# Kernel optimization log

Measured on AMD Instinct MI355X. Metric: run time of the kernel, lower is better.

The kernel has to match this reference:

```python
import jax, jax.numpy as jnp
import numpy as np

H = 128            # hardcoded image side in the torch module
TOL = 1e-3         # forward() default tol
MAX_DEPTH = 8      # init kwarg (reduced from 200 for bounded runtime)
LRELU = 0.1        # LeakyReLU negative slope


def _conv(x, w, b, pad):
    # x: [B,Cin,H,H], w: [Cout,Cin,kh,kw]
    y = jax.lax.conv_general_dilated(
        x, w, (1, 1), [(pad, pad), (pad, pad)],
        dimension_numbers=('NCHW', 'OIHW', 'NCHW'))
    if b is not None:
        y = y + b[None, :, None, None]
    return y


def _leaky(x):
    return jnp.where(x >= 0, x, LRELU * x)


def _build_apply_T(d, A, w1, b1, w2, b2, w3, b3, wK, delta, alpha, lambd, beta):
    B = d.shape[0]
    Kc = wK.shape[0]
    dcol = d.reshape(B, -1).T                      # [m, B]
    # ConvTranspose2d(K->1, k=3, pad=1) with weight := convK.weight is the
    # adjoint of convK: regular conv with spatially flipped, channel-swapped kernel.
    wKt = jnp.transpose(jnp.flip(wK, (2, 3)), (1, 0, 2, 3))  # [1,K,3,3]

    def K_op(xk):                                  # [N,B] -> [K*N,B]
        x4 = xk.T.reshape(B, 1, H, H)
        return _conv(x4, wK, None, 1).reshape(B, -1).T

    def Kt_op(pk):                                 # [K*N,B] -> [N,B]
        p4 = pk.T.reshape(B, Kc, H, H)
        return _conv(p4, wKt, None, 1).reshape(B, -1).T

    def R_op(pk):                                  # learned residual denoiser
        p = pk.T.reshape(B, Kc, H, H)
        p = p + _leaky(_conv(p, w1, b1, 2))
        p = p + _leaky(_conv(p, w2, b2, 2))
        p = p + _leaky(_conv(p, w3, b3, 2))
        return p.reshape(B, -1).T

    def ball_proj(w):                              # eval-mode projection
        de = jnp.exp(delta)                        # (1,) -> broadcasts over batch
        dist = jnp.maximum(jnp.linalg.norm(w - dcol, axis=0), 1e-10)
        dn = jnp.linalg.norm(dcol, axis=0)
        scale = jnp.minimum(jnp.ones_like(dist), de * dn / dist)
        return dcol + scale * (w - dcol)

    a = jnp.clip(alpha, 0.0, 2.0)
    bta = jnp.clip(beta, 0.0, 2.0)
    lam = jnp.clip(lambd, 0.0, 2.0)

    def apply_T(x):                                # x: [B,1,H,H]
        xk = x.reshape(B, -1).T                    # [N,B]
        Kxk = K_op(xk)
        # torch: pk = K(xk); pk += lambd*(nuk1 + alpha*(K(xk)-pk)) with nuk1=0
        # and pk==K(xk), so the update is identity -> pk = Kxk.
        pk = R_op(Kxk)
        Axk = A @ xk                               # [m,B]
        # torch: wk = A@xk; temp = wk + lambd*(nuk2 + alpha*(Axk-wk)) = Axk.
        wk = ball_proj(Axk)
        nuk1p = a * (Kxk - pk)
        nuk2p = a * (Axk - wk)
        # nuk1 = nuk2 = 0, so 2*nuk_plus - nuk = 2*nuk_plus
        rk = Kt_op(2.0 * nuk1p) + A.T @ (2.0 * nuk2p)
        xk_new = jnp.clip(xk - bta * rk, 0.0, 1.0)
        return xk_new.T.reshape(B, 1, H, H)

    return apply_T


def setup_inputs() -> dict:
    key = jax.random.key(0)
    ks = jax.random.split(key, 10)
    B, M, N_side, Kc = 8, 4096, 128, 2
    d = jax.random.normal(ks[0], (B, M), jnp.float32)
    A = jax.random.normal(ks[1], (M, N_side * N_side), jnp.float32) / 128.0
    w1 = jax.random.normal(ks[2], (Kc, Kc, 5, 5), jnp.float32) * 0.05
    w2 = jax.random.normal(ks[3], (Kc, Kc, 5, 5), jnp.float32) * 0.05
    w3 = jax.random.normal(ks[4], (Kc, Kc, 5, 5), jnp.float32) * 0.05
    b1 = jnp.zeros((Kc,), jnp.float32)
    b2 = jnp.zeros((Kc,), jnp.float32)
    b3 = jnp.zeros((Kc,), jnp.float32)
    wK = jax.random.normal(ks[5], (Kc, 1, 3, 3), jnp.float32) * 0.1
    return {
        'd': d, 'A': A,
        'w1': w1, 'b1': b1, 'w2': w2, 'b2': b2, 'w3': w3, 'b3': b3,
        'wK': wK,
        'delta': jnp.full((1,), -5.0, jnp.float32),
        'alpha': jnp.full((1,), 0.1, jnp.float32),
        'lambd': jnp.full((1,), 0.1, jnp.float32),
        'beta': jnp.full((1,), 0.1, jnp.float32),
    }


def reference(d, A, w1, b1, w2, b2, w3, b3, wK, delta, alpha, lambd, beta):
    B = d.shape[0]
    apply_T = _build_apply_T(d, A, w1, b1, w2, b2, w3, b3, wK,
                             delta, alpha, lambd, beta)
    x0 = jnp.zeros((B, 1, H, H), d.dtype)
    xp0 = jnp.full((B, 1, H, H), jnp.inf, d.dtype)

    def cond(state):
        x, xp, k = state
        res = jnp.max(jnp.linalg.norm((x - xp).reshape(B, -1), axis=1))
        return (res > TOL) & (k < MAX_DEPTH)

    def body(state):
        x, xp, k = state
        return (apply_T(x), x, k + 1)

    x_star, _, _ = jax.lax.while_loop(cond, body, (x0, xp0, jnp.int32(0)))
    # final differentiable application T(x*)
    return apply_T(x_star)
```

## Files before the change

### kernel.cpp

```cpp
#include <hip/hip_runtime.h>
#include <math.h>

#define HH 128
#define NPIX 16384
#define BB 8
#define MM 4096
#define NN 16384
#define LRELU_S 0.1f

typedef __attribute__((ext_vector_type(8))) short bf16x8;
typedef __attribute__((ext_vector_type(4))) float f32x4;

__device__ __forceinline__ float leaky_(float v){ return v >= 0.f ? v : LRELU_S*v; }
__device__ __forceinline__ float clamp01(float v){ return fminf(fmaxf(v, 0.f), 1.f); }
__device__ __forceinline__ float clamp02(float v){ return fminf(fmaxf(v, 0.f), 2.f); }
__device__ __forceinline__ unsigned short f2bf(float f){
  unsigned u = __float_as_uint(f);
  u = (u + 0x7FFFu + ((u >> 16) & 1u)) >> 16;
  return (unsigned short)u;
}
__device__ __forceinline__ float bf2f(unsigned short s){
  return __uint_as_float(((unsigned)s) << 16);
}

__global__ __launch_bounds__(256) void k_prep_both(const float* __restrict__ A_,
                                                   unsigned short* __restrict__ Abf,
                                                   unsigned short* __restrict__ Apk){
  __shared__ unsigned short lb[16][1032];
  int blk = blockIdx.x;
  int mt = blk >> 4, ch = blk & 15;
  int t = threadIdx.x;
  #pragma unroll
  for (int i=0;i<16;++i){
    float4 v = *(const float4*)&A_[(size_t)(mt*16+i)*NN + ch*1024 + t*4];
    unsigned short o[4] = {f2bf(v.x),f2bf(v.y),f2bf(v.z),f2bf(v.w)};
    *(uint2*)&lb[i][t*4] = *(uint2*)o;
    *(uint2*)&Abf[(size_t)(mt*16+i)*NN + ch*1024 + t*4] = *(uint2*)o;
  }
  __syncthreads();
  size_t base = ((size_t)mt*2048 + ch*128)*128;
  #pragma unroll
  for (int j=0;j<8;++j){
    int o = j*256 + t;
    int k8l = o >> 4, col = o & 15;
    uint4 v = *(const uint4*)&lb[col][k8l*8];
    *(uint4*)&Apk[base + (size_t)o*8] = v;
  }
}

__global__ __launch_bounds__(256) void k_dn(const float* __restrict__ d, float* __restrict__ dn){
  int b = blockIdx.x, t = threadIdx.x;
  float ss = 0.f;
  for (int m=t; m<MM; m+=256){ float v = d[b*MM + m]; ss += v*v; }
  #pragma unroll
  for (int off=32; off; off>>=1) ss += __shfl_down(ss, off);
  __shared__ float red[4];
  if ((t & 63) == 0) red[t>>6] = ss;
  __syncthreads();
  if (t == 0) dn[b] = sqrtf(red[0]+red[1]+red[2]+red[3]);
}

__global__ __launch_bounds__(256) void k_gemm1p(const unsigned short* __restrict__ Apk,
    const unsigned short* __restrict__ xtt, float* __restrict__ e_part){
  __shared__ float part[4][16][16];
  int blk = blockIdx.x;
  int mt = blk >> 2, ng = blk & 3;
  int t = threadIdx.x, w = t >> 6, lane = t & 63;
  int kg = lane >> 4, col = lane & 15;
  const unsigned short* Ap = Apk + (((size_t)mt*2048 + ng*512 + w*128 + kg)*16 + col)*8;
  const unsigned short* Bp = xtt + ((size_t)(ng*512 + w*128 + kg)*16 + col)*8;
  f32x4 acc = {0.f,0.f,0.f,0.f};
  #pragma unroll 8
  for (int s=0; s<32; ++s){
    bf16x8 a = *(const bf16x8*)(Ap + s*512);
    bf16x8 b = *(const bf16x8*)(Bp + s*512);
    acc = __builtin_amdgcn_mfma_f32_16x16x32_bf16(a, b, acc, 0, 0, 0);
  }
  #pragma unroll
  for (int j=0;j<4;++j) part[w][kg*4+j][col] = acc[j];
  __syncthreads();
  int r = t >> 4, b = t & 15;
  float s = part[0][r][b] + part[1][r][b] + part[2][r][b] + part[3][r][b];
  e_part[((size_t)ng*MM + mt*16 + r)*16 + b] = s;
}

__global__ __launch_bounds__(256) void k_conv_chain(const float* __restrict__ x,
    const float* __restrict__ wK, const float* __restrict__ w1, const float* __restrict__ b1,
    const float* __restrict__ w2, const float* __restrict__ b2,
    const float* __restrict__ w3, const float* __restrict__ b3,
    const float* __restrict__ alpha, float* __restrict__ rk){
  __shared__ float xs[24][128];
  __shared__ float bufA[2][22][128];
  __shared__ float bufB[2][18][128];
  __shared__ float wKs[18], w1s[100], w2s[100], w3s[100], bs[3][2];
  __shared__ float twoa;
  int blk = blockIdx.x;
  int b = blk >> 4, slab = blk & 15, r0 = slab*8;
  int t = threadIdx.x;
  for (int i=t;i<18;i+=256) wKs[i]=wK[i];
  for (int i=t;i<100;i+=256){ w1s[i]=w1[i]; w2s[i]=w2[i]; w3s[i]=w3[i]; }
  if (t<2){ bs[0][t]=b1[t]; bs[1][t]=b2[t]; bs[2][t]=b3[t]; }
  if (t==0) twoa = 2.f*clamp02(alpha[0]);
  for (int idx=t; idx<24*128; idx+=256){
    int i = idx>>7, j = idx&127, ir = r0-8+i;
    xs[i][j] = ((unsigned)ir < 128u) ? x[b*NPIX + ir*HH + j] : 0.f;
  }
  __syncthreads();
  for (int c=0;c<2;++c)
    for (int idx=t; idx<22*128; idx+=256){
      int i = idx>>7, j = idx&127, ir = r0-7+i;
      float s = 0.f;
      if ((unsigned)ir < 128u){
        #pragma unroll
        for (int di=0;di<3;++di)
          #pragma unroll
          for (int dj=0;dj<3;++dj){
            int jj = j+dj-1;
            if ((unsigned)jj < 128u) s += xs[i+di][jj]*wKs[(c*3+di)*3+dj];
          }
      }
      bufA[c][i][j] = s;
    }
  __syncthreads();
  for (int o=0;o<2;++o)
    for (int idx=t; idx<18*128; idx+=256){
      int i = idx>>7, j = idx&127, ir = r0-5+i;
      float v = 0.f;
      if ((unsigned)ir < 128u){
        float s = bs[0][o];
        #pragma unroll
        for (int c=0;c<2;++c)
          #pragma unroll
          for (int di=0;di<5;++di)
            #pragma unroll
            for (int dj=0;dj<5;++dj){
              int jj = j+dj-2;
              if ((unsigned)jj < 128u) s += bufA[c][i+di][jj]*w1s[(o*2+c)*25+di*5+dj];
            }
        v = bufA[o][i+2][j] + leaky_(s);
      }
      bufB[o][i][j] = v;
    }
  __syncthreads();
  for (int o=0;o<2;++o)
    for (int idx=t; idx<14*128; idx+=256){
      int i = idx>>7, j = idx&127, ir = r0-3+i;
      float v = 0.f;
      if ((unsigned)ir < 128u){
        float s = bs[1][o];
        #pragma unroll
        for (int c=0;c<2;++c)
          #pragma unroll
          for (int di=0;di<5;++di)
            #pragma unroll
            for (int dj=0;dj<5;++dj){
              int jj = j+dj-2;
              if ((unsigned)jj < 128u) s += bufB[c][i+di][jj]*w2s[(o*2+c)*25+di*5+dj];
            }
        v = bufB[o][i+2][j] + leaky_(s);
      }
      bufA[o][i][j] = v;
    }
  __syncthreads();
  for (int o=0;o<2;++o)
    for (int idx=t; idx<10*128; idx+=256){
      int i = idx>>7, j = idx&127, ir = r0-1+i;
      float v = 0.f;
      if ((unsigned)ir < 128u){
        float s = bs[2][o];
        #pragma unroll
        for (int c=0;c<2;++c)
          #pragma unroll
          for (int di=0;di<5;++di)
            #pragma unroll
            for (int dj=0;dj<5;++dj){
              int jj = j+dj-2;
              if ((unsigned)jj < 128u) s += bufA[c][i+di][jj]*w3s[(o*2+c)*25+di*5+dj];
            }
        v = bufA[o][i+2][j] + leaky_(s);
      }
      bufB[o][i][j] = v;
    }
  __syncthreads();
  for (int c=0;c<2;++c)
    for (int idx=t; idx<10*128; idx+=256){
      int i = idx>>7, j = idx&127, ir = r0-1+i;
      float v = 0.f;
      if ((unsigned)ir < 128u){
        float kx = 0.f;
        #pragma unroll
        for (int di=0;di<3;++di)
          #pragma unroll
          for (int dj=0;dj<3;++dj){
            int jj = j+dj-1;
            if ((unsigned)jj < 128u) kx += xs[i+6+di][jj]*wKs[(c*3+di)*3+dj];
          }
        v = twoa*(kx - bufB[c][i][j]);
      }
      bufA[c][i][j] = v;
    }
  __syncthreads();
  for (int idx=t; idx<8*128; idx+=256){
    int i = idx>>7, j = idx&127, ir = r0+i;
    float s = 0.f;
    #pragma unroll
    for (int c=0;c<2;++c)
      #pragma unroll
      for (int di=0;di<3;++di)
        #pragma unroll
        for (int dj=0;dj<3;++dj){
          int jj = j+dj-1;
          if ((unsigned)jj < 128u) s += bufA[c][i+di][jj]*wKs[(c*3+(2-di))*3+(2-dj)];
        }
    rk[b*NPIX + ir*HH + j] = s;
  }
}

__global__ __launch_bounds__(256) void k_gemm2n(const unsigned short* __restrict__ Abf,
    const float* __restrict__ e_part, const float* __restrict__ d_,
    float* __restrict__ up, float* __restrict__ d2p){
  __shared__ float zs[8][128];
  __shared__ float red8s[64];
  int blk = blockIdx.x;
  int ms = blk >> 5, nb = blk & 31;
  int m0 = ms*128, n0 = nb*512;
  int t = threadIdx.x;
  for (int i=t; i<1024; i+=256){
    int ml = i >> 3, b = i & 7;
    int m = m0 + ml;
    float s = e_part[(size_t)(0*MM + m)*16 + b]
            + e_part[(size_t)(1*MM + m)*16 + b]
            + e_part[(size_t)(2*MM + m)*16 + b]
            + e_part[(size_t)(3*MM + m)*16 + b];
    zs[b][ml] = s - d_[b*MM + m];
  }
  __syncthreads();
  if (nb == 0){
    if (t < 64){
      int b = t & 7, g = t >> 3;
      float s = 0.f;
      #pragma unroll
      for (int i=0;i<16;++i){ float v = zs[b][g*16+i]; s += v*v; }
      red8s[g*8 + b] = s;
    }
    __syncthreads();
    if (t < 8){
      float s2 = 0.f;
      #pragma unroll
      for (int g=0;g<8;++g) s2 += red8s[g*8 + t];
      d2p[ms*8 + t] = s2;
    }
  }
  int c = t & 127, h = t >> 7;
  const unsigned short* Ap = Abf + (size_t)(m0 + h*64)*NN + n0 + c*4;
  float acc[4][8];
  #pragma unroll
  for (int e=0;e<4;++e)
    #pragma unroll
    for (int b=0;b<8;++b) acc[e][b] = 0.f;
  for (int mo=0; mo<64; mo+=8){
    uint2 a8[8];
    #pragma unroll
    for (int u=0;u<8;++u) a8[u] = *(const uint2*)(Ap + (size_t)(mo+u)*NN);
    #pragma unroll
    for (int u=0;u<8;++u){
      float av0 = bf2f((unsigned short)(a8[u].x & 0xffff));
      float av1 = bf2f((unsigned short)(a8[u].x >> 16));
      float av2 = bf2f((unsigned short)(a8[u].y & 0xffff));
      float av3 = bf2f((unsigned short)(a8[u].y >> 16));
      int ml = h*64 + mo + u;
      #pragma unroll
      for (int b=0;b<8;++b){
        float z = zs[b][ml];
        acc[0][b] += av0*z; acc[1][b] += av1*z;
        acc[2][b] += av2*z; acc[3][b] += av3*z;
      }
    }
  }
  int pg = ms*2 + h;
  #pragma unroll
  for (int b=0;b<8;++b){
    float4 v = {acc[0][b], acc[1][b], acc[2][b], acc[3][b]};
    *(float4*)&up[((size_t)pg*8 + b)*NN + n0 + c*4] = v;
  }
}

__global__ __launch_bounds__(256) void k_combine3(const float* __restrict__ up,
    const float* __restrict__ rk1, const float* __restrict__ d2p,
    const float* __restrict__ dn, const float* __restrict__ delta,
    const float* __restrict__ alpha, const float* __restrict__ beta,
    float* __restrict__ x, unsigned short* __restrict__ xtt){
  __shared__ float cf_s[8];
  int t = threadIdx.x;
  if (t < 8){
    float s2 = 0.f;
    #pragma unroll
    for (int ms=0; ms<32; ++ms) s2 += d2p[ms*8 + t];
    float dist = fmaxf(sqrtf(s2), 1e-10f);
    float de = expf(delta[0]);
    float a = clamp02(alpha[0]);
    cf_s[t] = 2.f*a*(1.f - fminf(1.f, de*dn[t]/dist));
  }
  __syncthreads();
  float bta = clamp02(beta[0]);
  int o = blockIdx.x*256 + t;
  int b = o >> 14, pix = o & 16383;
  float s = 0.f;
  #pragma unroll
  for (int p=0; p<64; ++p)
    s += up[((size_t)p*8 + b)*NN + pix];
  float tot = rk1[b*NPIX + pix] + cf_s[b]*s;
  float xn = clamp01(x[b*NPIX + pix] - bta*tot);
  x[b*NPIX + pix] = xn;
  xtt[((size_t)(pix>>3)*16 + b)*8 + (pix&7)] = f2bf(xn);
}

extern "C" void kernel_launch(void* const* d_in, const int* in_sizes, int n_in,
                              void* d_out, int out_size, void* d_ws, size_t ws_size,
                              hipStream_t stream) {
  const float* d_d   = (const float*)d_in[0];
  const float* d_A   = (const float*)d_in[1];
  const float* w1    = (const float*)d_in[2];
  const float* b1    = (const float*)d_in[3];
  const float* w2    = (const float*)d_in[4];
  const float* b2    = (const float*)d_in[5];
  const float* w3    = (const float*)d_in[6];
  const float* b3    = (const float*)d_in[7];
  const float* wK    = (const float*)d_in[8];
  const float* delta = (const float*)d_in[9];
  const float* alpha = (const float*)d_in[10];
  const float* beta  = (const float*)d_in[12];

  char* p = (char*)d_ws;
  unsigned short* Abf = (unsigned short*)p; p += (size_t)MM*NN*2;
  unsigned short* Apk = (unsigned short*)p; p += (size_t)MM*NN*2;
  unsigned short* xtt = (unsigned short*)p; p += (size_t)2048*16*8*2;
  float* x      = (float*)p; p += (size_t)BB*NPIX*4;
  float* rk1    = (float*)p; p += (size_t)BB*NPIX*4;
  float* e_part = (float*)p; p += (size_t)4*MM*16*4;
  float* up     = (float*)p; p += (size_t)64*8*NN*4;
  float* d2p    = (float*)p; p += (size_t)32*8*4;
  float* dnb    = (float*)p; p += 64;

  k_prep_both<<<4096, 256, 0, stream>>>(d_A, Abf, Apk);
  k_dn<<<BB, 256, 0, stream>>>(d_d, dnb);
  hipMemsetAsync(x, 0, (size_t)BB*NPIX*4, stream);
  hipMemsetAsync(xtt, 0, (size_t)2048*16*8*2, stream);

  for (int it=0; it<9; ++it){
    k_conv_chain<<<128, 256, 0, stream>>>(x, wK, w1, b1, w2, b2, w3, b3, alpha, rk1);
    k_gemm1p<<<1024, 256, 0, stream>>>(Apk, xtt, e_part);
    k_gemm2n<<<1024, 256, 0, stream>>>(Abf, e_part, d_d, up, d2p);
    k_combine3<<<512, 256, 0, stream>>>(up, rk1, d2p, dnb, delta, alpha, beta, x, xtt);
  }

  hipMemcpyAsync(d_out, x, (size_t)BB*NPIX*4, hipMemcpyDeviceToDevice, stream);
}
```

Measured before the change: 1.595 ms.

## Reuse packed A layout for transpose GEMM and drop row-major bf16 copy

The A^T·z GEMM now reads the same packed bf16 layout that the forward GEMM uses, so the separate row-major bf16 copy of A no longer has to be written during prep. Each block covers 512 rows of m and 64 output columns, reducing partials across lanes with xor shuffles. This shrinks the partial-sum buffer from 64 to 8 slices, which cuts traffic in the combine kernel. The cost is shuffle-reduction work, and the strided packed loads may coalesce less well than the old row-major reads.

```diff
diff --git a/kernel.cpp b/kernel.cpp
--- a/kernel.cpp
+++ b/kernel.cpp
@@ -23,8 +23,7 @@
   return __uint_as_float(((unsigned)s) << 16);
 }
 
-__global__ __launch_bounds__(256) void k_prep_both(const float* __restrict__ A_,
-                                                   unsigned short* __restrict__ Abf,
+__global__ __launch_bounds__(256) void k_prep_pack(const float* __restrict__ A_,
                                                    unsigned short* __restrict__ Apk){
   __shared__ unsigned short lb[16][1032];
   int blk = blockIdx.x;
@@ -35,7 +34,6 @@
     float4 v = *(const float4*)&A_[(size_t)(mt*16+i)*NN + ch*1024 + t*4];
     unsigned short o[4] = {f2bf(v.x),f2bf(v.y),f2bf(v.z),f2bf(v.w)};
     *(uint2*)&lb[i][t*4] = *(uint2*)o;
-    *(uint2*)&Abf[(size_t)(mt*16+i)*NN + ch*1024 + t*4] = *(uint2*)o;
   }
   __syncthreads();
   size_t base = ((size_t)mt*2048 + ch*128)*128;
@@ -216,16 +214,16 @@
   }
 }
 
-__global__ __launch_bounds__(256) void k_gemm2n(const unsigned short* __restrict__ Abf,
+__global__ __launch_bounds__(256) void k_gemm2a(const unsigned short* __restrict__ Apk,
     const float* __restrict__ e_part, const float* __restrict__ d_,
     float* __restrict__ up, float* __restrict__ d2p){
-  __shared__ float zs[8][128];
+  __shared__ float zs[8][512];
   __shared__ float red8s[64];
   int blk = blockIdx.x;
-  int ms = blk >> 5, nb = blk & 31;
-  int m0 = ms*128, n0 = nb*512;
+  int msp = blk >> 8, nb = blk & 255;
+  int m0 = msp*512, mt0 = msp*32, k80 = nb*8;
   int t = threadIdx.x;
-  for (int i=t; i<1024; i+=256){
+  for (int i=t; i<4096; i+=256){
     int ml = i >> 3, b = i & 7;
     int m = m0 + ml;
     float s = e_part[(size_t)(0*MM + m)*16 + b]
@@ -240,7 +238,7 @@
       int b = t & 7, g = t >> 3;
       float s = 0.f;
       #pragma unroll
-      for (int i=0;i<16;++i){ float v = zs[b][g*16+i]; s += v*v; }
+      for (int i=0;i<64;++i){ float v = zs[b][g*64+i]; s += v*v; }
       red8s[g*8 + b] = s;
     }
     __syncthreads();
@@ -248,40 +246,48 @@
       float s2 = 0.f;
       #pragma unroll
       for (int g=0;g<8;++g) s2 += red8s[g*8 + t];
-      d2p[ms*8 + t] = s2;
-    }
-  }
-  int c = t & 127, h = t >> 7;
-  const unsigned short* Ap = Abf + (size_t)(m0 + h*64)*NN + n0 + c*4;
-  float acc[4][8];
-  #pragma unroll
-  for (int e=0;e<4;++e)
-    #pragma unroll
-    for (int b=0;b<8;++b) acc[e][b] = 0.f;
-  for (int mo=0; mo<64; mo+=8){
-    uint2 a8[8];
-    #pragma unroll
-    for (int u=0;u<8;++u) a8[u] = *(const uint2*)(Ap + (size_t)(mo+u)*NN);
-    #pragma unroll
-    for (int u=0;u<8;++u){
-      float av0 = bf2f((unsigned short)(a8[u].x & 0xffff));
-      float av1 = bf2f((unsigned short)(a8[u].x >> 16));
-      float av2 = bf2f((unsigned short)(a8[u].y & 0xffff));
-      float av3 = bf2f((unsigned short)(a8[u].y >> 16));
-      int ml = h*64 + mo + u;
+      d2p[msp*8 + t] = s2;
+    }
+  }
+  int col = t & 15, ehalf = (t >> 4) & 1, k8l = t >> 5;
+  int k8 = k80 + k8l;
+  const unsigned short* Ap = Apk + ((((size_t)mt0*2048 + k8)*16 + col)*8 + ehalf*4);
+  float acc[8][4];
+  #pragma unroll
+  for (int b=0;b<8;++b)
+    #pragma unroll
+    for (int e=0;e<4;++e) acc[b][e] = 0.f;
+  for (int mb=0; mb<32; mb+=4){
+    uint2 a4[4];
+    #pragma unroll
+    for (int u=0;u<4;++u)
+      a4[u] = *(const uint2*)(Ap + (size_t)(mb+u)*262144);
+    #pragma unroll
+    for (int u=0;u<4;++u){
+      float av[4];
+      av[0] = bf2f((unsigned short)(a4[u].x & 0xffff));
+      av[1] = bf2f((unsigned short)(a4[u].x >> 16));
+      av[2] = bf2f((unsigned short)(a4[u].y & 0xffff));
+      av[3] = bf2f((unsigned short)(a4[u].y >> 16));
+      int ml = (mb+u)*16 + col;
       #pragma unroll
       for (int b=0;b<8;++b){
         float z = zs[b][ml];
-        acc[0][b] += av0*z; acc[1][b] += av1*z;
-        acc[2][b] += av2*z; acc[3][b] += av3*z;
-      }
-    }
-  }
-  int pg = ms*2 + h;
-  #pragma unroll
-  for (int b=0;b<8;++b){
-    float4 v = {acc[0][b], acc[1][b], acc[2][b], acc[3][b]};
-    *(float4*)&up[((size_t)pg*8 + b)*NN + n0 + c*4] = v;
+        acc[b][0] += av[0]*z; acc[b][1] += av[1]*z;
+        acc[b][2] += av[2]*z; acc[b][3] += av[3]*z;
+      }
+    }
+  }
+  #pragma unroll
+  for (int mask=1; mask<16; mask<<=1)
+    #pragma unroll
+    for (int b=0;b<8;++b)
+      #pragma unroll
+      for (int e=0;e<4;++e) acc[b][e] += __shfl_xor(acc[b][e], mask);
+  if (col < 8){
+    int b = col;
+    float4 v = {acc[b][0], acc[b][1], acc[b][2], acc[b][3]};
+    *(float4*)&up[((size_t)msp*8 + b)*NN + k8*8 + ehalf*4] = v;
   }
 }
 
@@ -295,7 +301,7 @@
   if (t < 8){
     float s2 = 0.f;
     #pragma unroll
-    for (int ms=0; ms<32; ++ms) s2 += d2p[ms*8 + t];
+    for (int ms=0; ms<8; ++ms) s2 += d2p[ms*8 + t];
     float dist = fmaxf(sqrtf(s2), 1e-10f);
     float de = expf(delta[0]);
     float a = clamp02(alpha[0]);
@@ -307,7 +313,7 @@
   int b = o >> 14, pix = o & 16383;
   float s = 0.f;
   #pragma unroll
-  for (int p=0; p<64; ++p)
+  for (int p=0; p<8; ++p)
     s += up[((size_t)p*8 + b)*NN + pix];
   float tot = rk1[b*NPIX + pix] + cf_s[b]*s;
   float xn = clamp01(x[b*NPIX + pix] - bta*tot);
@@ -332,17 +338,16 @@
   const float* beta  = (const float*)d_in[12];
 
   char* p = (char*)d_ws;
-  unsigned short* Abf = (unsigned short*)p; p += (size_t)MM*NN*2;
   unsigned short* Apk = (unsigned short*)p; p += (size_t)MM*NN*2;
   unsigned short* xtt = (unsigned short*)p; p += (size_t)2048*16*8*2;
   float* x      = (float*)p; p += (size_t)BB*NPIX*4;
   float* rk1    = (float*)p; p += (size_t)BB*NPIX*4;
   float* e_part = (float*)p; p += (size_t)4*MM*16*4;
-  float* up     = (float*)p; p += (size_t)64*8*NN*4;
-  float* d2p    = (float*)p; p += (size_t)32*8*4;
+  float* up     = (float*)p; p += (size_t)8*8*NN*4;
+  float* d2p    = (float*)p; p += (size_t)8*8*4;
   float* dnb    = (float*)p; p += 64;
 
-  k_prep_both<<<4096, 256, 0, stream>>>(d_A, Abf, Apk);
+  k_prep_pack<<<4096, 256, 0, stream>>>(d_A, Apk);
   k_dn<<<BB, 256, 0, stream>>>(d_d, dnb);
   hipMemsetAsync(x, 0, (size_t)BB*NPIX*4, stream);
   hipMemsetAsync(xtt, 0, (size_t)2048*16*8*2, stream);
@@ -350,7 +355,7 @@
   for (int it=0; it<9; ++it){
     k_conv_chain<<<128, 256, 0, stream>>>(x, wK, w1, b1, w2, b2, w3, b3, alpha, rk1);
     k_gemm1p<<<1024, 256, 0, stream>>>(Apk, xtt, e_part);
-    k_gemm2n<<<1024, 256, 0, stream>>>(Abf, e_part, d_d, up, d2p);
+    k_gemm2a<<<2048, 256, 0, stream>>>(Apk, e_part, d_d, up, d2p);
     k_combine3<<<512, 256, 0, stream>>>(up, rk1, d2p, dnb, delta, alpha, beta, x, xtt);
   }
 
```

Measured after the change: 1.492 ms. -6.4%, faster.

## Replace scalar A^T z GEMM with bf16 MFMA kernel on pre-transposed A

Applied to the files above, without the earlier changes.

The second GEMM (A^T times the residual z) moves from scalar FMA over a row-major bf16 copy of A to MFMA 16x16x32 bf16 instructions. It reads a new k-packed transposed copy of A built once at setup, with z packed to bf16 by a separate small kernel. The partial-sum buffer shrinks from 64 partials to 2, so the combine kernel reads far less. This adds a transpose prep pass and a kernel launch per iteration, and rounds z to bf16, which may cost some accuracy.

```diff
diff --git a/kernel.cpp b/kernel.cpp
--- a/kernel.cpp
+++ b/kernel.cpp
@@ -23,8 +23,7 @@
   return __uint_as_float(((unsigned)s) << 16);
 }
 
-__global__ __launch_bounds__(256) void k_prep_both(const float* __restrict__ A_,
-                                                   unsigned short* __restrict__ Abf,
+__global__ __launch_bounds__(256) void k_prep_pack(const float* __restrict__ A_,
                                                    unsigned short* __restrict__ Apk){
   __shared__ unsigned short lb[16][1032];
   int blk = blockIdx.x;
@@ -35,7 +34,6 @@
     float4 v = *(const float4*)&A_[(size_t)(mt*16+i)*NN + ch*1024 + t*4];
     unsigned short o[4] = {f2bf(v.x),f2bf(v.y),f2bf(v.z),f2bf(v.w)};
     *(uint2*)&lb[i][t*4] = *(uint2*)o;
-    *(uint2*)&Abf[(size_t)(mt*16+i)*NN + ch*1024 + t*4] = *(uint2*)o;
   }
   __syncthreads();
   size_t base = ((size_t)mt*2048 + ch*128)*128;
@@ -45,6 +43,26 @@
     int k8l = o >> 4, col = o & 15;
     uint4 v = *(const uint4*)&lb[col][k8l*8];
     *(uint4*)&Apk[base + (size_t)o*8] = v;
+  }
+}
+
+__global__ __launch_bounds__(256) void k_prep_atp(const float* __restrict__ A_,
+                                                  unsigned short* __restrict__ Atp){
+  __shared__ float lds[64][65];
+  int bm = blockIdx.x >> 8, bn = blockIdx.x & 255;
+  int m0 = bm*64, n0 = bn*64;
+  int t = threadIdx.x;
+  for (int i=t; i<64*16; i+=256){
+    int r = i >> 4, c4 = i & 15;
+    float4 v = *(const float4*)&A_[(size_t)(m0+r)*NN + n0 + c4*4];
+    lds[r][c4*4+0]=v.x; lds[r][c4*4+1]=v.y; lds[r][c4*4+2]=v.z; lds[r][c4*4+3]=v.w;
+  }
+  __syncthreads();
+  for (int i=t; i<8*64; i+=256){
+    int mbl = i >> 6, nl = i & 63;
+    unsigned short o[8];
+    for (int j=0;j<8;++j) o[j] = f2bf(lds[mbl*8+j][nl]);
+    *(uint4*)&Atp[((size_t)(m0/8 + mbl)*NN + n0 + nl)*8] = *(uint4*)o;
   }
 }
 
@@ -216,14 +234,13 @@
   }
 }
 
-__global__ __launch_bounds__(256) void k_gemm2n(const unsigned short* __restrict__ Abf,
-    const float* __restrict__ e_part, const float* __restrict__ d_,
-    float* __restrict__ up, float* __restrict__ d2p){
+__global__ __launch_bounds__(256) void k_zt2(const float* __restrict__ e_part,
+    const float* __restrict__ d_, unsigned short* __restrict__ zt,
+    float* __restrict__ d2p){
   __shared__ float zs[8][128];
   __shared__ float red8s[64];
   int blk = blockIdx.x;
-  int ms = blk >> 5, nb = blk & 31;
-  int m0 = ms*128, n0 = nb*512;
+  int m0 = blk*128;
   int t = threadIdx.x;
   for (int i=t; i<1024; i+=256){
     int ml = i >> 3, b = i & 7;
@@ -235,57 +252,48 @@
     zs[b][ml] = s - d_[b*MM + m];
   }
   __syncthreads();
-  if (nb == 0){
-    if (t < 64){
-      int b = t & 7, g = t >> 3;
-      float s = 0.f;
-      #pragma unroll
-      for (int i=0;i<16;++i){ float v = zs[b][g*16+i]; s += v*v; }
-      red8s[g*8 + b] = s;
-    }
-    __syncthreads();
-    if (t < 8){
-      float s2 = 0.f;
-      #pragma unroll
-      for (int g=0;g<8;++g) s2 += red8s[g*8 + t];
-      d2p[ms*8 + t] = s2;
-    }
-  }
-  int c = t & 127, h = t >> 7;
-  const unsigned short* Ap = Abf + (size_t)(m0 + h*64)*NN + n0 + c*4;
-  float acc[4][8];
-  #pragma unroll
-  for (int e=0;e<4;++e)
+  if (t < 64){
+    int b = t & 7, g = t >> 3;
+    float s = 0.f;
     #pragma unroll
-    for (int b=0;b<8;++b) acc[e][b] = 0.f;
-  for (int mo=0; mo<64; mo+=8){
-    uint2 a8[8];
+    for (int i=0;i<16;++i){ float v = zs[b][g*16+i]; s += v*v; }
+    red8s[g*8 + b] = s;
+  }
+  __syncthreads();
+  if (t < 8){
+    float s2 = 0.f;
     #pragma unroll
-    for (int u=0;u<8;++u) a8[u] = *(const uint2*)(Ap + (size_t)(mo+u)*NN);
-    #pragma unroll
-    for (int u=0;u<8;++u){
-      float av0 = bf2f((unsigned short)(a8[u].x & 0xffff));
-      float av1 = bf2f((unsigned short)(a8[u].x >> 16));
-      float av2 = bf2f((unsigned short)(a8[u].y & 0xffff));
-      float av3 = bf2f((unsigned short)(a8[u].y >> 16));
-      int ml = h*64 + mo + u;
-      #pragma unroll
-      for (int b=0;b<8;++b){
-        float z = zs[b][ml];
-        acc[0][b] += av0*z; acc[1][b] += av1*z;
-        acc[2][b] += av2*z; acc[3][b] += av3*z;
-      }
-    }
-  }
-  int pg = ms*2 + h;
-  #pragma unroll
-  for (int b=0;b<8;++b){
-    float4 v = {acc[0][b], acc[1][b], acc[2][b], acc[3][b]};
-    *(float4*)&up[((size_t)pg*8 + b)*NN + n0 + c*4] = v;
-  }
-}
-
-__global__ __launch_bounds__(256) void k_combine3(const float* __restrict__ up,
+    for (int g=0;g<8;++g) s2 += red8s[g*8 + t];
+    d2p[blk*8 + t] = s2;
+  }
+  for (int idx=t; idx<128*16; idx+=256){
+    int ml = idx >> 4, b = idx & 15, m = m0 + ml;
+    float v = (b < 8) ? zs[b][ml] : 0.f;
+    zt[(size_t)(m>>3)*128 + b*8 + (m&7)] = f2bf(v);
+  }
+}
+
+__global__ __launch_bounds__(64) void k_g2m(const unsigned short* __restrict__ Atp,
+    const unsigned short* __restrict__ zt, float* __restrict__ up){
+  int blk = blockIdx.x;
+  int nt = blk >> 1, ms = blk & 1;
+  int lane = threadIdx.x;
+  int kg = lane >> 4, nc = lane & 15;
+  const unsigned short* Ap = zt  + ((size_t)(ms*256 + kg)*16 + nc)*8;
+  const unsigned short* Bp = Atp + ((size_t)(ms*256 + kg)*NN + nt*16 + nc)*8;
+  f32x4 acc = {0.f,0.f,0.f,0.f};
+  #pragma unroll 8
+  for (int s=0; s<64; ++s){
+    bf16x8 a = *(const bf16x8*)(Ap + (size_t)s*512);
+    bf16x8 b = *(const bf16x8*)(Bp + (size_t)s*4*NN*8);
+    acc = __builtin_amdgcn_mfma_f32_16x16x32_bf16(a, b, acc, 0, 0, 0);
+  }
+  #pragma unroll
+  for (int j=0;j<4;++j)
+    up[(size_t)(ms*16 + kg*4 + j)*NN + nt*16 + nc] = acc[j];
+}
+
+__global__ __launch_bounds__(256) void k_combine4(const float* __restrict__ up,
     const float* __restrict__ rk1, const float* __restrict__ d2p,
     const float* __restrict__ dn, const float* __restrict__ delta,
     const float* __restrict__ alpha, const float* __restrict__ beta,
@@ -305,10 +313,7 @@
   float bta = clamp02(beta[0]);
   int o = blockIdx.x*256 + t;
   int b = o >> 14, pix = o & 16383;
-  float s = 0.f;
-  #pragma unroll
-  for (int p=0; p<64; ++p)
-    s += up[((size_t)p*8 + b)*NN + pix];
+  float s = up[(size_t)(0*16 + b)*NN + pix] + up[(size_t)(1*16 + b)*NN + pix];
   float tot = rk1[b*NPIX + pix] + cf_s[b]*s;
   float xn = clamp01(x[b*NPIX + pix] - bta*tot);
   x[b*NPIX + pix] = xn;
@@ -332,17 +337,19 @@
   const float* beta  = (const float*)d_in[12];
 
   char* p = (char*)d_ws;
-  unsigned short* Abf = (unsigned short*)p; p += (size_t)MM*NN*2;
   unsigned short* Apk = (unsigned short*)p; p += (size_t)MM*NN*2;
+  unsigned short* Atp = (unsigned short*)p; p += (size_t)MM*NN*2;
   unsigned short* xtt = (unsigned short*)p; p += (size_t)2048*16*8*2;
+  unsigned short* zt  = (unsigned short*)p; p += (size_t)512*16*8*2;
   float* x      = (float*)p; p += (size_t)BB*NPIX*4;
   float* rk1    = (float*)p; p += (size_t)BB*NPIX*4;
   float* e_part = (float*)p; p += (size_t)4*MM*16*4;
-  float* up     = (float*)p; p += (size_t)64*8*NN*4;
+  float* up     = (float*)p; p += (size_t)2*16*NN*4;
   float* d2p    = (float*)p; p += (size_t)32*8*4;
   float* dnb    = (float*)p; p += 64;
 
-  k_prep_both<<<4096, 256, 0, stream>>>(d_A, Abf, Apk);
+  k_prep_pack<<<4096, 256, 0, stream>>>(d_A, Apk);
+  k_prep_atp<<<64*256, 256, 0, stream>>>(d_A, Atp);
   k_dn<<<BB, 256, 0, stream>>>(d_d, dnb);
   hipMemsetAsync(x, 0, (size_t)BB*NPIX*4, stream);
   hipMemsetAsync(xtt, 0, (size_t)2048*16*8*2, stream);
@@ -350,8 +357,9 @@
   for (int it=0; it<9; ++it){
     k_conv_chain<<<128, 256, 0, stream>>>(x, wK, w1, b1, w2, b2, w3, b3, alpha, rk1);
     k_gemm1p<<<1024, 256, 0, stream>>>(Apk, xtt, e_part);
-    k_gemm2n<<<1024, 256, 0, stream>>>(Abf, e_part, d_d, up, d2p);
-    k_combine3<<<512, 256, 0, stream>>>(up, rk1, d2p, dnb, delta, alpha, beta, x, xtt);
+    k_zt2<<<32, 256, 0, stream>>>(e_part, d_d, zt, d2p);
+    k_g2m<<<2048, 64, 0, stream>>>(Atp, zt, up);
+    k_combine4<<<512, 256, 0, stream>>>(up, rk1, d2p, dnb, delta, alpha, beta, x, xtt);
   }
 
   hipMemcpyAsync(d_out, x, (size_t)BB*NPIX*4, hipMemcpyDeviceToDevice, stream);
```

Measured after the change: 1.448 ms. 1.1x faster.
